# Kernel optimization log

Measured on AMD Instinct MI355X. Metric: run time of the kernel, lower is better.

## Reference

```python
import jax, jax.numpy as jnp
import numpy as np
import math

B, S, D_MODEL = 4, 2048, 1024
H, D_QK, D_V = 16, 64, 64


def setup_inputs() -> dict:
    key = jax.random.key(0)
    ks = jax.random.split(key, 12)
    s = 0.02
    return {
        "input_q": jax.random.normal(ks[0], (B, S, D_MODEL), jnp.float32),
        "input_k": jax.random.normal(ks[1], (B, S, D_MODEL), jnp.float32),
        "input_v": jax.random.normal(ks[2], (B, S, D_MODEL), jnp.float32),
        # per-head projection weights stacked over heads: [H, out, d_model] (torch Linear layout)
        "WQw": jax.random.normal(ks[3], (H, D_QK, D_MODEL), jnp.float32) * s,
        "WQb": jax.random.normal(ks[4], (H, D_QK), jnp.float32) * s,
        "WKw": jax.random.normal(ks[5], (H, D_QK, D_MODEL), jnp.float32) * s,
        "WKb": jax.random.normal(ks[6], (H, D_QK), jnp.float32) * s,
        "WVw": jax.random.normal(ks[7], (H, D_V, D_MODEL), jnp.float32) * s,
        "WVb": jax.random.normal(ks[8], (H, D_V), jnp.float32) * s,
        # output projection: Linear(H*D_V, D_MODEL)
        "Ww": jax.random.normal(ks[9], (D_MODEL, H * D_V), jnp.float32) * s,
        "Wb": jax.random.normal(ks[10], (D_MODEL,), jnp.float32) * s,
    }


def _mha(input_q, input_k, input_v, WQw, WQb, WKw, WKb, WVw, WVb, Ww, Wb):
    # per-head projections: [B,H,S,d]
    Q = jnp.einsum("bsd,hed->bhse", input_q, WQw) + WQb[None, :, None, :]
    K = jnp.einsum("bsd,hed->bhse", input_k, WKw) + WKb[None, :, None, :]
    V = jnp.einsum("bsd,hvd->bhsv", input_v, WVw) + WVb[None, :, None, :]
    scores = jnp.einsum("bhse,bhte->bhst", Q, K)  # [B,H,S,S]
    # causal mask added BEFORE division by sqrt(d_model), as in original
    causal = jnp.triu(jnp.full((S, S), -jnp.inf, scores.dtype), k=1)
    scores = (scores + causal) / math.sqrt(D_MODEL)  # NOTE: d_model, not d_qk
    attn = jax.nn.softmax(scores, axis=-1)
    ctx = jnp.einsum("bhst,bhtv->bhsv", attn, V)  # [B,H,S,D_V]
    concat = ctx.transpose(0, 2, 1, 3).reshape(B, S, H * D_V)  # head-order concat
    return concat @ Ww.T + Wb


def reference(input_q, input_k, input_v, WQw, WQb, WKw, WKb, WVw, WVb, Ww, Wb):
    return _mha(input_q, input_k, input_v, WQw, WQb, WKw, WKb, WVw, WVb, Ww, Wb)
```

## Files before the change

### kernel.cpp

```cpp
#include <hip/hip_runtime.h>
#include <hip/hip_bf16.h>

typedef __attribute__((ext_vector_type(8))) short bf16x8;
typedef __attribute__((ext_vector_type(4))) float f32x4;
typedef __attribute__((ext_vector_type(16))) float f32x16;
typedef __attribute__((ext_vector_type(4))) unsigned uint4v;

#define MFMA16(a, b, c) __builtin_amdgcn_mfma_f32_16x16x32_bf16(a, b, c, 0, 0, 0)
#define MFMA32(a, b, c) __builtin_amdgcn_mfma_f32_32x32x16_bf16(a, b, c, 0, 0, 0)

__device__ __forceinline__ unsigned short f2bfn(float f) {
#if defined(__gfx950__)
  __bf16 h = (__bf16)f;
  return __builtin_bit_cast(unsigned short, h);
#else
  union { float f; unsigned u; } x; x.f = f;
  unsigned r = x.u + 0x7fffu + ((x.u >> 16) & 1u);
  return (unsigned short)(r >> 16);
#endif
}

__device__ __forceinline__ unsigned cvtpk(float lo, float hi) {
  unsigned w;
  asm("v_cvt_pk_bf16_f32 %0, %1, %2" : "=v"(w) : "v"(lo), "v"(hi));
  return w;
}

__device__ __forceinline__ void cvt_range(const float* __restrict__ s,
                                          unsigned short* __restrict__ d,
                                          int i, int st, int n8) {
  for (; i < n8; i += st) {
    const float4* sp = reinterpret_cast<const float4*>(s) + 2 * (size_t)i;
    float4 a = sp[0], b = sp[1];
    uint4v o;
    o[0] = cvtpk(a.x, a.y); o[1] = cvtpk(a.z, a.w);
    o[2] = cvtpk(b.x, b.y); o[3] = cvtpk(b.z, b.w);
    reinterpret_cast<uint4v*>(d)[i] = o;
  }
}

__global__ void cvt1_kernel(const float* __restrict__ s, unsigned short* __restrict__ d, int n8) {
  cvt_range(s, d, blockIdx.x * blockDim.x + threadIdx.x, gridDim.x * blockDim.x, n8);
}

__global__ void cvt_first_kernel(const float* s0, const float* s1, const float* s2,
                                 const float* s3, unsigned short* d0, unsigned short* d1,
                                 unsigned short* d2, unsigned short* d3, int wn8,
                                 const float* sq, unsigned short* dq, int qn8) {
  const float* s; unsigned short* d; int n8;
  switch (blockIdx.y) {
    case 0: s = s0; d = d0; n8 = wn8; break;
    case 1: s = s1; d = d1; n8 = wn8; break;
    case 2: s = s2; d = d2; n8 = wn8; break;
    case 3: s = s3; d = d3; n8 = wn8; break;
    default: s = sq; d = dq; n8 = qn8; break;
  }
  cvt_range(s, d, blockIdx.x * blockDim.x + threadIdx.x, gridDim.x * blockDim.x, n8);
}

template <int MODE>
__global__ __launch_bounds__(256) void gemm_kernel(
    const unsigned short* __restrict__ Av, const unsigned short* __restrict__ Bv,
    const float* __restrict__ bias, void* __restrict__ outv,
    int M, int N, int K, float oscale, int nshift, int ngemm,
    const float* __restrict__ csrc, unsigned short* __restrict__ cdst, int cn8) {
  constexpr int BM = 128, BN = 128, BK = 64;
  __shared__ __align__(16) unsigned short As[2][BM * BK];
  __shared__ __align__(16) unsigned short Bs[2][BN * BK];
  const int bx = blockIdx.x;
  const int tid = threadIdx.x;
  if (bx >= ngemm) {
    cvt_range(csrc, cdst, (bx - ngemm) * blockDim.x + tid,
              (gridDim.x - ngemm) * blockDim.x, cn8);
    return;
  }
  const int lane = tid & 63, wave = tid >> 6;
  const int wr = wave >> 1, wc = wave & 1;
  const int m0 = (bx >> nshift) * BM, n0 = (bx & ((1 << nshift) - 1)) * BN;
  const int rb = lane & 15, g = lane >> 4;
  const int swz = ((lane & 7) ^ ((lane >> 3) & 7)) * 8;
  f32x4 acc[4][4] = {};

  const unsigned short* Ab = Av + (size_t)m0 * K;
  const unsigned short* Bb = Bv + (size_t)n0 * K;

  auto stage = [&](int buf, int k0) {
#pragma unroll
    for (int i = 0; i < 4; ++i) {
      const int c = wave * 256 + i * 64 + lane;
      const int r = c >> 3;
      __builtin_amdgcn_global_load_lds(
          (const __attribute__((address_space(1))) unsigned int*)(Ab + (size_t)r * K + k0 + swz),
          (__attribute__((address_space(3))) unsigned int*)&As[buf][c * 8], 16, 0, 0);
      __builtin_amdgcn_global_load_lds(
          (const __attribute__((address_space(1))) unsigned int*)(Bb + (size_t)r * K + k0 + swz),
          (__attribute__((address_space(3))) unsigned int*)&Bs[buf][c * 8], 16, 0, 0);
    }
  };

  const int nt = K / BK;
  stage(0, 0);
  int cur = 0;
  for (int t = 0; t < nt; ++t) {
    __syncthreads();
    if (t + 1 < nt) stage(cur ^ 1, (t + 1) * BK);
    const unsigned short* A_ = As[cur];
    const unsigned short* B_ = Bs[cur];
#pragma unroll
    for (int kc = 0; kc < 2; ++kc) {
      bf16x8 af[4], bfr[4];
#pragma unroll
      for (int mi = 0; mi < 4; ++mi)
        af[mi] = *reinterpret_cast<const bf16x8*>(
            &A_[(wr * 64 + mi * 16 + rb) * 64 + (((kc * 4 + g) ^ (rb & 7)) * 8)]);
#pragma unroll
      for (int ni = 0; ni < 4; ++ni)
        bfr[ni] = *reinterpret_cast<const bf16x8*>(
            &B_[(wc * 64 + ni * 16 + rb) * 64 + (((kc * 4 + g) ^ (rb & 7)) * 8)]);
#pragma unroll
      for (int mi = 0; mi < 4; ++mi)
#pragma unroll
        for (int ni = 0; ni < 4; ++ni)
          acc[mi][ni] = MFMA16(af[mi], bfr[ni], acc[mi][ni]);
    }
    cur ^= 1;
  }

#pragma unroll
  for (int mi = 0; mi < 4; ++mi) {
#pragma unroll
    for (int ni = 0; ni < 4; ++ni) {
      int col = n0 + wc * 64 + ni * 16 + rb;
      if constexpr (MODE != 2) {
        float bv = bias[col];
#pragma unroll
        for (int j = 0; j < 4; ++j) {
          int row = m0 + wr * 64 + mi * 16 + g * 4 + j;
          float v = acc[mi][ni][j] + bv;
          if constexpr (MODE == 0) {
            v *= oscale;
            int b = row >> 11, s = row & 2047;
            int h = col >> 6, e = col & 63;
            ((unsigned short*)outv)[((size_t)(b * 16 + h) * 2048 + s) * 64 + e] = f2bfn(v);
          } else {
            ((float*)outv)[(size_t)row * N + col] = v;
          }
        }
      } else {
        int bb = col >> 11, s = col & 2047;
#pragma unroll
        for (int j = 0; j < 4; ++j) {
          int row = m0 + wr * 64 + mi * 16 + g * 4 + j;
          float v = acc[mi][ni][j] + bias[row];
          int h = row >> 6, e = row & 63;
          ((unsigned short*)outv)[((size_t)(bb * 16 + h) * 64 + e) * 2048 + s] = f2bfn(v);
        }
      }
    }
  }
}

__global__ __launch_bounds__(256) void attn7_kernel(
    const unsigned short* __restrict__ Qp, const unsigned short* __restrict__ Kp,
    const unsigned short* __restrict__ Vtp, unsigned short* __restrict__ ctx) {
  constexpr int S = 2048;
  __shared__ __align__(16) unsigned short Ks[2][64 * 64];
  __shared__ __align__(16) unsigned short Vs[2][64 * 64];
  const int bx = blockIdx.x;
  const int bh = bx & 63;
  const int qti = 15 - (bx >> 6);
  const int tid = threadIdx.x, wave = tid >> 6, lane = tid & 63;
  const int l31 = lane & 31, hb = lane >> 5;
  const int x7 = l31 & 7;
  const int qw = qti * 128 + wave * 32;
  const unsigned short* Qb = Qp + (size_t)bh * S * 64;
  const unsigned short* Kb = Kp + (size_t)bh * S * 64;
  const unsigned short* Vb = Vtp + (size_t)bh * 64 * S;

  bf16x8 qg[4];
#pragma unroll
  for (int kc = 0; kc < 4; ++kc)
    qg[kc] = *reinterpret_cast<const bf16x8*>(
        Qb + (size_t)(qw + l31) * 64 + 16 * kc + 8 * hb);

  bf16x8 ones;
#pragma unroll
  for (int i = 0; i < 8; ++i) ones[i] = (short)0x3F80;

  f32x16 ls = {};
  f32x16 o[2] = {};
  const int sswz = ((lane & 7) ^ (lane >> 3)) * 8;
  const int nt = qti * 2 + 2;

  const int ci0 = wave * 2 * 64 + lane, ci1 = ci0 + 64;
  const int r0 = wave * 16 + (lane >> 3), r1 = r0 + 8;
  const int rs0 = (r0 & 51) | ((r0 & 4) << 1) | ((r0 & 8) >> 1);
  const int rs1 = (r1 & 51) | ((r1 & 4) << 1) | ((r1 & 8) >> 1);
  const unsigned short* ks0 = Kb + (size_t)rs0 * 64 + sswz;
  const unsigned short* ks1 = Kb + (size_t)rs1 * 64 + sswz;
  const unsigned short* vs0 = Vb + (size_t)r0 * S + sswz;
  const unsigned short* vs1 = Vb + (size_t)r1 * S + sswz;

  auto stage = [&](int buf) {
    __builtin_amdgcn_global_load_lds(
        (const __attribute__((address_space(1))) unsigned int*)ks0,
        (__attribute__((address_space(3))) unsigned int*)&Ks[buf][ci0 * 8], 16, 0, 0);
    __builtin_amdgcn_global_load_lds(
        (const __attribute__((address_space(1))) unsigned int*)ks1,
        (__attribute__((address_space(3))) unsigned int*)&Ks[buf][ci1 * 8], 16, 0, 0);
    __builtin_amdgcn_global_load_lds(
        (const __attribute__((address_space(1))) unsigned int*)vs0,
        (__attribute__((address_space(3))) unsigned int*)&Vs[buf][ci0 * 8], 16, 0, 0);
    __builtin_amdgcn_global_load_lds(
        (const __attribute__((address_space(1))) unsigned int*)vs1,
        (__attribute__((address_space(3))) unsigned int*)&Vs[buf][ci1 * 8], 16, 0, 0);
    ks0 += 4096; ks1 += 4096;
    vs0 += 64; vs1 += 64;
  };

  stage(0);

  for (int it = 0; it < nt; ++it) {
    __syncthreads();
    if (it + 1 < nt) stage((it + 1) & 1);
    const int kv0 = 64 * it;
    if (kv0 <= qw + 31) {
      const unsigned short* K_ = Ks[it & 1];
      const unsigned short* V_ = Vs[it & 1];
      f32x16 sacc[2] = {};
      __builtin_amdgcn_s_setprio(1);
#pragma unroll
      for (int kc = 0; kc < 4; ++kc) {
        bf16x8 kf0 = *reinterpret_cast<const bf16x8*>(
            &K_[l31 * 64 + ((2 * kc + hb) ^ x7) * 8]);
        bf16x8 kf1 = *reinterpret_cast<const bf16x8*>(
            &K_[(32 + l31) * 64 + ((2 * kc + hb) ^ x7) * 8]);
        sacc[0] = MFMA32(kf0, qg[kc], sacc[0]);
        sacc[1] = MFMA32(kf1, qg[kc], sacc[1]);
      }
      __builtin_amdgcn_s_setprio(0);
      if (kv0 + 63 > qw) {
        const int qrel = qw + l31 - kv0 - 8 * hb;
#pragma unroll
        for (int mi = 0; mi < 2; ++mi)
#pragma unroll
          for (int r = 0; r < 16; ++r) {
            int koff = (r & 7) + 16 * (r >> 3) + 32 * mi;
            if (koff > qrel) sacc[mi][r] = -1e30f;
          }
      }
      float p0[16], p1[16];
#pragma unroll
      for (int r = 0; r < 16; ++r) p0[r] = __builtin_amdgcn_exp2f(sacc[0][r]);
#pragma unroll
      for (int r = 0; r < 16; ++r) p1[r] = __builtin_amdgcn_exp2f(sacc[1][r]);
      unsigned pw[2][8];
#pragma unroll
      for (int i = 0; i < 8; ++i) pw[0][i] = cvtpk(p0[2 * i], p0[2 * i + 1]);
#pragma unroll
      for (int i = 0; i < 8; ++i) pw[1][i] = cvtpk(p1[2 * i], p1[2 * i + 1]);
      __builtin_amdgcn_s_setprio(1);
#pragma unroll
      for (int c = 0; c < 4; ++c) {
        union { unsigned u[4]; bf16x8 v; } pu;
        pu.u[0] = pw[c >> 1][(c & 1) * 4 + 0];
        pu.u[1] = pw[c >> 1][(c & 1) * 4 + 1];
        pu.u[2] = pw[c >> 1][(c & 1) * 4 + 2];
        pu.u[3] = pw[c >> 1][(c & 1) * 4 + 3];
#pragma unroll
        for (int db = 0; db < 2; ++db) {
          bf16x8 vf = *reinterpret_cast<const bf16x8*>(
              &V_[(32 * db + l31) * 64 + ((2 * c + hb) ^ x7) * 8]);
          o[db] = MFMA32(vf, pu.v, o[db]);
        }
        ls = MFMA32(ones, pu.v, ls);
      }
      __builtin_amdgcn_s_setprio(0);
    }
  }

  const float inv = 1.0f / ls[0];
  const int b = bh >> 4, h = bh & 15;
  const int q = qw + l31;
  unsigned short* cp = ctx + ((size_t)(b * 2048 + q) * 1024) + h * 64;
#pragma unroll
  for (int db = 0; db < 2; ++db)
#pragma unroll
    for (int i = 0; i < 8; ++i) {
      unsigned w = cvtpk(o[db][2 * i] * inv, o[db][2 * i + 1] * inv);
      int d = 32 * db + ((2 * i) & 3) + 8 * (i >> 1) + 4 * hb;
      *reinterpret_cast<unsigned*>(cp + d) = w;
    }
}

extern "C" void kernel_launch(void* const* d_in, const int* in_sizes, int n_in,
                              void* d_out, int out_size, void* d_ws, size_t ws_size,
                              hipStream_t stream) {
  const float* in_q = (const float*)d_in[0];
  const float* in_k = (const float*)d_in[1];
  const float* in_v = (const float*)d_in[2];
  const float* WQw = (const float*)d_in[3];
  const float* WQb = (const float*)d_in[4];
  const float* WKw = (const float*)d_in[5];
  const float* WKb = (const float*)d_in[6];
  const float* WVw = (const float*)d_in[7];
  const float* WVb = (const float*)d_in[8];
  const float* Ww  = (const float*)d_in[9];
  const float* Wb  = (const float*)d_in[10];
  float* out = (float*)d_out;

  constexpr size_t PROJ = (size_t)4 * 16 * 2048 * 64;
  constexpr size_t WSZ = (size_t)1024 * 1024;
  const float qscale = 0.03125f * 1.4426950408889634f;
  unsigned short* wsp = (unsigned short*)d_ws;

  const bool fused = ws_size >= (6 * PROJ + 4 * WSZ) * sizeof(unsigned short);

  if (fused) {
    unsigned short* Qp   = wsp;
    unsigned short* Kp   = wsp + PROJ;
    unsigned short* Vt   = wsp + 2 * PROJ;
    unsigned short* inq  = wsp + 3 * PROJ;
    unsigned short* ctx  = inq;
    unsigned short* ink  = wsp + 4 * PROJ;
    unsigned short* inv  = wsp + 5 * PROJ;
    unsigned short* wq16 = wsp + 6 * PROJ;
    unsigned short* wk16 = wq16 + WSZ;
    unsigned short* wv16 = wk16 + WSZ;
    unsigned short* ww16 = wv16 + WSZ;

    cvt_first_kernel<<<dim3(1024, 5), 256, 0, stream>>>(
        WQw, WKw, WVw, Ww, wq16, wk16, wv16, ww16, (int)(WSZ / 8),
        in_q, inq, (int)(PROJ / 8));
    gemm_kernel<0><<<2560, 256, 0, stream>>>(inq, wq16, WQb, Qp, 8192, 1024, 1024,
                                             qscale, 3, 512, in_k, ink, (int)(PROJ / 8));
    gemm_kernel<0><<<2560, 256, 0, stream>>>(ink, wk16, WKb, Kp, 8192, 1024, 1024,
                                             1.0f, 3, 512, in_v, inv, (int)(PROJ / 8));
    gemm_kernel<2><<<512, 256, 0, stream>>>(wv16, inv, WVb, Vt, 1024, 8192, 1024,
                                            1.0f, 6, 512, nullptr, nullptr, 0);
    attn7_kernel<<<1024, 256, 0, stream>>>(Qp, Kp, Vt, ctx);
    gemm_kernel<1><<<512, 256, 0, stream>>>(ctx, ww16, Wb, out, 8192, 1024, 1024,
                                            1.0f, 3, 512, nullptr, nullptr, 0);
  } else {
    unsigned short* Qp   = wsp;
    unsigned short* Kp   = wsp + PROJ;
    unsigned short* Vt   = wsp + 2 * PROJ;
    unsigned short* in16 = wsp + 3 * PROJ;
    unsigned short* ctx  = in16;
    unsigned short* wq16 = wsp + 4 * PROJ;
    unsigned short* wk16 = wq16 + WSZ;
    unsigned short* wv16 = wk16 + WSZ;
    unsigned short* ww16 = wv16 + WSZ;

    cvt_first_kernel<<<dim3(1024, 5), 256, 0, stream>>>(
        WQw, WKw, WVw, Ww, wq16, wk16, wv16, ww16, (int)(WSZ / 8),
        in_q, in16, (int)(PROJ / 8));
    gemm_kernel<0><<<512, 256, 0, stream>>>(in16, wq16, WQb, Qp, 8192, 1024, 1024,
                                            qscale, 3, 512, nullptr, nullptr, 0);
    cvt1_kernel<<<2048, 256, 0, stream>>>(in_k, in16, (int)(PROJ / 8));
    gemm_kernel<0><<<512, 256, 0, stream>>>(in16, wk16, WKb, Kp, 8192, 1024, 1024,
                                            1.0f, 3, 512, nullptr, nullptr, 0);
    cvt1_kernel<<<2048, 256, 0, stream>>>(in_v, in16, (int)(PROJ / 8));
    gemm_kernel<2><<<512, 256, 0, stream>>>(wv16, in16, WVb, Vt, 1024, 8192, 1024,
                                            1.0f, 6, 512, nullptr, nullptr, 0);
    attn7_kernel<<<1024, 256, 0, stream>>>(Qp, Kp, Vt, ctx);
    gemm_kernel<1><<<512, 256, 0, stream>>>(ctx, ww16, Wb, out, 8192, 1024, 1024,
                                            1.0f, 3, 512, nullptr, nullptr, 0);
  }
}
```

Before: 184.0 us.

## Merge Q/K/V projection GEMMs into one launch and convert all inputs upfront

Converts all three fp32 inputs and all weights to bf16 in a single launch, then runs the Q, K and V projection GEMMs as one 1536-block grid that picks its operands by block index. This replaces the earlier scheme where conversion work for the next input was folded into the previous GEMM's grid. The aim is fewer launches and a fuller device, since the three independent GEMMs can run concurrently instead of as 512-block launches in sequence. The trade-off is that no GEMM can start until every input has been converted, so conversion no longer overlaps with compute. The fallback path is also reworked but still runs its GEMMs separately.

```diff
diff --git a/kernel.cpp b/kernel.cpp
--- a/kernel.cpp
+++ b/kernel.cpp
@@ -43,40 +43,47 @@
   cvt_range(s, d, blockIdx.x * blockDim.x + threadIdx.x, gridDim.x * blockDim.x, n8);
 }
 
-__global__ void cvt_first_kernel(const float* s0, const float* s1, const float* s2,
-                                 const float* s3, unsigned short* d0, unsigned short* d1,
-                                 unsigned short* d2, unsigned short* d3, int wn8,
-                                 const float* sq, unsigned short* dq, int qn8) {
+__global__ void cvt_all_kernel(const float* s0, const float* s1, const float* s2,
+                               const float* s3, unsigned short* d0, unsigned short* d1,
+                               unsigned short* d2, unsigned short* d3, int wn8,
+                               const float* a0, const float* a1, const float* a2,
+                               unsigned short* e0, unsigned short* e1, unsigned short* e2,
+                               int an8) {
   const float* s; unsigned short* d; int n8;
   switch (blockIdx.y) {
     case 0: s = s0; d = d0; n8 = wn8; break;
     case 1: s = s1; d = d1; n8 = wn8; break;
     case 2: s = s2; d = d2; n8 = wn8; break;
     case 3: s = s3; d = d3; n8 = wn8; break;
-    default: s = sq; d = dq; n8 = qn8; break;
+    case 4: s = a0; d = e0; n8 = an8; break;
+    case 5: s = a1; d = e1; n8 = an8; break;
+    default: s = a2; d = e2; n8 = an8; break;
   }
   cvt_range(s, d, blockIdx.x * blockDim.x + threadIdx.x, gridDim.x * blockDim.x, n8);
 }
 
-template <int MODE>
-__global__ __launch_bounds__(256) void gemm_kernel(
-    const unsigned short* __restrict__ Av, const unsigned short* __restrict__ Bv,
-    const float* __restrict__ bias, void* __restrict__ outv,
-    int M, int N, int K, float oscale, int nshift, int ngemm,
-    const float* __restrict__ csrc, unsigned short* __restrict__ cdst, int cn8) {
-  constexpr int BM = 128, BN = 128, BK = 64;
-  __shared__ __align__(16) unsigned short As[2][BM * BK];
-  __shared__ __align__(16) unsigned short Bs[2][BN * BK];
+__global__ __launch_bounds__(256) void gemm_qkv_kernel(
+    const unsigned short* __restrict__ inq, const unsigned short* __restrict__ ink,
+    const unsigned short* __restrict__ invv, const unsigned short* __restrict__ wq,
+    const unsigned short* __restrict__ wk, const unsigned short* __restrict__ wv,
+    const float* __restrict__ bq, const float* __restrict__ bk,
+    const float* __restrict__ bv, unsigned short* __restrict__ Qp,
+    unsigned short* __restrict__ Kp, unsigned short* __restrict__ Vt, float qscale) {
+  constexpr int K = 1024, BK = 64;
+  __shared__ __align__(16) unsigned short As[2][128 * BK];
+  __shared__ __align__(16) unsigned short Bs[2][128 * BK];
   const int bx = blockIdx.x;
+  const int mode = bx >> 9;
+  const int pm = bx & 511;
   const int tid = threadIdx.x;
-  if (bx >= ngemm) {
-    cvt_range(csrc, cdst, (bx - ngemm) * blockDim.x + tid,
-              (gridDim.x - ngemm) * blockDim.x, cn8);
-    return;
-  }
   const int lane = tid & 63, wave = tid >> 6;
   const int wr = wave >> 1, wc = wave & 1;
-  const int m0 = (bx >> nshift) * BM, n0 = (bx & ((1 << nshift) - 1)) * BN;
+  const unsigned short *Av, *Bv;
+  const float* bias;
+  int m0, n0;
+  if (mode == 0)      { Av = inq; Bv = wq; bias = bq; m0 = (pm >> 3) * 128; n0 = (pm & 7) * 128; }
+  else if (mode == 1) { Av = ink; Bv = wk; bias = bk; m0 = (pm >> 3) * 128; n0 = (pm & 7) * 128; }
+  else                { Av = wv; Bv = invv; bias = bv; m0 = (pm >> 6) * 128; n0 = (pm & 63) * 128; }
   const int rb = lane & 15, g = lane >> 4;
   const int swz = ((lane & 7) ^ ((lane >> 3) & 7)) * 8;
   f32x4 acc[4][4] = {};
@@ -98,6 +105,103 @@
     }
   };
 
+  stage(0, 0);
+  int cur = 0;
+  for (int t = 0; t < K / BK; ++t) {
+    __syncthreads();
+    if (t + 1 < K / BK) stage(cur ^ 1, (t + 1) * BK);
+    const unsigned short* A_ = As[cur];
+    const unsigned short* B_ = Bs[cur];
+#pragma unroll
+    for (int kc = 0; kc < 2; ++kc) {
+      bf16x8 af[4], bfr[4];
+#pragma unroll
+      for (int mi = 0; mi < 4; ++mi)
+        af[mi] = *reinterpret_cast<const bf16x8*>(
+            &A_[(wr * 64 + mi * 16 + rb) * 64 + (((kc * 4 + g) ^ (rb & 7)) * 8)]);
+#pragma unroll
+      for (int ni = 0; ni < 4; ++ni)
+        bfr[ni] = *reinterpret_cast<const bf16x8*>(
+            &B_[(wc * 64 + ni * 16 + rb) * 64 + (((kc * 4 + g) ^ (rb & 7)) * 8)]);
+#pragma unroll
+      for (int mi = 0; mi < 4; ++mi)
+#pragma unroll
+        for (int ni = 0; ni < 4; ++ni)
+          acc[mi][ni] = MFMA16(af[mi], bfr[ni], acc[mi][ni]);
+    }
+    cur ^= 1;
+  }
+
+  if (mode < 2) {
+    unsigned short* outp = (mode == 0) ? Qp : Kp;
+    const float osc = (mode == 0) ? qscale : 1.0f;
+#pragma unroll
+    for (int mi = 0; mi < 4; ++mi)
+#pragma unroll
+      for (int ni = 0; ni < 4; ++ni) {
+        int col = n0 + wc * 64 + ni * 16 + rb;
+        float bvv = bias[col];
+#pragma unroll
+        for (int j = 0; j < 4; ++j) {
+          int row = m0 + wr * 64 + mi * 16 + g * 4 + j;
+          float v = (acc[mi][ni][j] + bvv) * osc;
+          int b = row >> 11, s = row & 2047;
+          int h = col >> 6, e = col & 63;
+          outp[((size_t)(b * 16 + h) * 2048 + s) * 64 + e] = f2bfn(v);
+        }
+      }
+  } else {
+#pragma unroll
+    for (int mi = 0; mi < 4; ++mi)
+#pragma unroll
+      for (int ni = 0; ni < 4; ++ni) {
+        int col = n0 + wc * 64 + ni * 16 + rb;
+        int bb = col >> 11, s = col & 2047;
+#pragma unroll
+        for (int j = 0; j < 4; ++j) {
+          int row = m0 + wr * 64 + mi * 16 + g * 4 + j;
+          float v = acc[mi][ni][j] + bias[row];
+          int h = row >> 6, e = row & 63;
+          Vt[((size_t)(bb * 16 + h) * 64 + e) * 2048 + s] = f2bfn(v);
+        }
+      }
+  }
+}
+
+template <int MODE>
+__global__ __launch_bounds__(256) void gemm_kernel(
+    const unsigned short* __restrict__ Av, const unsigned short* __restrict__ Bv,
+    const float* __restrict__ bias, void* __restrict__ outv,
+    int M, int N, int K, float oscale, int nshift) {
+  constexpr int BK = 64;
+  __shared__ __align__(16) unsigned short As[2][128 * BK];
+  __shared__ __align__(16) unsigned short Bs[2][128 * BK];
+  const int bx = blockIdx.x;
+  const int tid = threadIdx.x;
+  const int lane = tid & 63, wave = tid >> 6;
+  const int wr = wave >> 1, wc = wave & 1;
+  const int m0 = (bx >> nshift) * 128, n0 = (bx & ((1 << nshift) - 1)) * 128;
+  const int rb = lane & 15, g = lane >> 4;
+  const int swz = ((lane & 7) ^ ((lane >> 3) & 7)) * 8;
+  f32x4 acc[4][4] = {};
+
+  const unsigned short* Ab = Av + (size_t)m0 * K;
+  const unsigned short* Bb = Bv + (size_t)n0 * K;
+
+  auto stage = [&](int buf, int k0) {
+#pragma unroll
+    for (int i = 0; i < 4; ++i) {
+      const int c = wave * 256 + i * 64 + lane;
+      const int r = c >> 3;
+      __builtin_amdgcn_global_load_lds(
+          (const __attribute__((address_space(1))) unsigned int*)(Ab + (size_t)r * K + k0 + swz),
+          (__attribute__((address_space(3))) unsigned int*)&As[buf][c * 8], 16, 0, 0);
+      __builtin_amdgcn_global_load_lds(
+          (const __attribute__((address_space(1))) unsigned int*)(Bb + (size_t)r * K + k0 + swz),
+          (__attribute__((address_space(3))) unsigned int*)&Bs[buf][c * 8], 16, 0, 0);
+    }
+  };
+
   const int nt = K / BK;
   stage(0, 0);
   int cur = 0;
@@ -132,11 +236,11 @@
     for (int ni = 0; ni < 4; ++ni) {
       int col = n0 + wc * 64 + ni * 16 + rb;
       if constexpr (MODE != 2) {
-        float bv = bias[col];
+        float bvv = bias[col];
 #pragma unroll
         for (int j = 0; j < 4; ++j) {
           int row = m0 + wr * 64 + mi * 16 + g * 4 + j;
-          float v = acc[mi][ni][j] + bv;
+          float v = acc[mi][ni][j] + bvv;
           if constexpr (MODE == 0) {
             v *= oscale;
             int b = row >> 11, s = row & 2047;
@@ -329,18 +433,14 @@
     unsigned short* wv16 = wk16 + WSZ;
     unsigned short* ww16 = wv16 + WSZ;
 
-    cvt_first_kernel<<<dim3(1024, 5), 256, 0, stream>>>(
+    cvt_all_kernel<<<dim3(512, 7), 256, 0, stream>>>(
         WQw, WKw, WVw, Ww, wq16, wk16, wv16, ww16, (int)(WSZ / 8),
-        in_q, inq, (int)(PROJ / 8));
-    gemm_kernel<0><<<2560, 256, 0, stream>>>(inq, wq16, WQb, Qp, 8192, 1024, 1024,
-                                             qscale, 3, 512, in_k, ink, (int)(PROJ / 8));
-    gemm_kernel<0><<<2560, 256, 0, stream>>>(ink, wk16, WKb, Kp, 8192, 1024, 1024,
-                                             1.0f, 3, 512, in_v, inv, (int)(PROJ / 8));
-    gemm_kernel<2><<<512, 256, 0, stream>>>(wv16, inv, WVb, Vt, 1024, 8192, 1024,
-                                            1.0f, 6, 512, nullptr, nullptr, 0);
+        in_q, in_k, in_v, inq, ink, inv, (int)(PROJ / 8));
+    gemm_qkv_kernel<<<1536, 256, 0, stream>>>(inq, ink, inv, wq16, wk16, wv16,
+                                              WQb, WKb, WVb, Qp, Kp, Vt, qscale);
     attn7_kernel<<<1024, 256, 0, stream>>>(Qp, Kp, Vt, ctx);
     gemm_kernel<1><<<512, 256, 0, stream>>>(ctx, ww16, Wb, out, 8192, 1024, 1024,
-                                            1.0f, 3, 512, nullptr, nullptr, 0);
+                                            1.0f, 3);
   } else {
     unsigned short* Qp   = wsp;
     unsigned short* Kp   = wsp + PROJ;
@@ -352,19 +452,20 @@
     unsigned short* wv16 = wk16 + WSZ;
     unsigned short* ww16 = wv16 + WSZ;
 
-    cvt_first_kernel<<<dim3(1024, 5), 256, 0, stream>>>(
+    cvt_all_kernel<<<dim3(512, 5), 256, 0, stream>>>(
         WQw, WKw, WVw, Ww, wq16, wk16, wv16, ww16, (int)(WSZ / 8),
-        in_q, in16, (int)(PROJ / 8));
+        in_q, in_q, in_q, in16, in16, in16, 0);
+    cvt1_kernel<<<2048, 256, 0, stream>>>(in_q, in16, (int)(PROJ / 8));
     gemm_kernel<0><<<512, 256, 0, stream>>>(in16, wq16, WQb, Qp, 8192, 1024, 1024,
-                                            qscale, 3, 512, nullptr, nullptr, 0);
+                                            qscale, 3);
     cvt1_kernel<<<2048, 256, 0, stream>>>(in_k, in16, (int)(PROJ / 8));
     gemm_kernel<0><<<512, 256, 0, stream>>>(in16, wk16, WKb, Kp, 8192, 1024, 1024,
-                                            1.0f, 3, 512, nullptr, nullptr, 0);
+                                            1.0f, 3);
     cvt1_kernel<<<2048, 256, 0, stream>>>(in_v, in16, (int)(PROJ / 8));
     gemm_kernel<2><<<512, 256, 0, stream>>>(wv16, in16, WVb, Vt, 1024, 8192, 1024,
-                                            1.0f, 6, 512, nullptr, nullptr, 0);
+                                            1.0f, 6);
     attn7_kernel<<<1024, 256, 0, stream>>>(Qp, Kp, Vt, ctx);
     gemm_kernel<1><<<512, 256, 0, stream>>>(ctx, ww16, Wb, out, 8192, 1024, 1024,
-                                            1.0f, 3, 512, nullptr, nullptr, 0);
-  }
-}
+                                            1.0f, 3);
+  }
+}
```

Result: no change. 185.8 us (+1.0%).
